# Performance work log

Hardware: AMD Instinct MI355X
Metric: run time of the kernel (lower is better)

The kernel has to match this reference:

```python
import math
import jax, jax.numpy as jnp
import numpy as np

C, H, W, N = 128, 64, 64, 32


def setup_inputs() -> dict:
    key = jax.random.key(0)
    k = jax.random.split(key, 6)
    std = 0.02
    return {
        "x": jax.random.normal(k[0], (N, C, H, W), dtype=jnp.float32),
        # p_3: 1x1 conv, weight [out=C, in=3C]
        "w3": jax.random.normal(k[1], (C, 3 * C), dtype=jnp.float32) * std,
        "p5_w": jax.random.normal(k[2], (1, 1, H, W), dtype=jnp.float32) * std,
        # p_6: conv (3,1), dilation (3,1), weight [O=C, I=C, 3, 1]
        "w6": jax.random.normal(k[3], (C, C, 3, 1), dtype=jnp.float32) * std,
        "p8_w": jax.random.normal(k[4], (1, C, 1, 1), dtype=jnp.float32) * std,
        "p12_w": jax.random.normal(k[5], (1, 1, 3, H, 1), dtype=jnp.float32) * std,
    }


def reference(x, w3, p5_w, w6, p8_w, p12_w):
    n, c, h, w = x.shape
    # F.unfold(x, (1,3), dilation=(1,2), padding=(0,2)) -> taps at w-2, w, w+2 (zero padded)
    xp = jnp.pad(x, ((0, 0), (0, 0), (0, 0), (2, 2)))
    t1 = jnp.stack([xp[..., 0:w], xp[..., 2:w + 2], xp[..., 4:w + 4]], axis=2)  # [n,c,3,h,w]
    t2 = t1.max(axis=2)                                                          # [n,c,h,w]
    # p_3: 1x1 conv over 3c channels
    t3 = jnp.einsum('nkhw,ok->nohw', t1.reshape(n, c * 3, h, w), w3)            # [n,c,h,w]
    t4 = jnp.maximum(t3[:, :, None], t1)                                         # [n,c,3,h,w]
    t5 = p5_w * t2
    # p_6: (3,1) conv, dilation (3,1), padding (3,0) -> same spatial size
    t6 = jax.lax.conv_general_dilated(
        t5, w6, window_strides=(1, 1), padding=((3, 3), (0, 0)),
        rhs_dilation=(3, 1), dimension_numbers=('NCHW', 'OIHW', 'NCHW'))         # [n,c,h,w]
    t7 = jnp.maximum(x, t6)
    t8 = p8_w * t7
    # bmm: [n,c,hw] x [n,hw,3c] -> [n,c,3c]
    t9 = jnp.einsum('ncp,nkp->nck', t8.reshape(n, c, h * w),
                    t1.reshape(n, c * 3, h * w)) / math.sqrt(h * w)
    t10 = t7[:, :, None] + t4                                                    # [n,c,3,h,w]
    t11 = jnp.maximum(t6[:, :, None], t10)                                       # [n,c,3,h,w]
    t12 = p12_w * t11
    # bmm: [n,hw,3c] x [n,3c,c] -> [n,hw,c]
    t13 = jnp.einsum('nkp,nck->npc', t12.reshape(n, c * 3, h * w), t9) / math.sqrt(c * 3)
    return t13.reshape(n, h, w, c).transpose(0, 3, 1, 2)                         # [n,c,h,w]
```

## Files before the change

### kernel.cpp

```cpp
#include <hip/hip_runtime.h>

#define C_   128
#define P_   4096
#define K3   384
#define CP   (C_*P_)
#define NB_  32

typedef __attribute__((ext_vector_type(8))) short short8;
typedef __attribute__((ext_vector_type(4))) short short4v;
typedef __attribute__((ext_vector_type(4))) float f32x4;

__device__ __forceinline__ short f2bf(float f) {
  union { float f; unsigned u; } v; v.f = f;
  unsigned r = v.u + 0x7fffu + ((v.u >> 16) & 1u);
  return (short)(r >> 16);
}
__device__ __forceinline__ float bf2f(short b) {
  union { unsigned u; float f; } v; v.u = ((unsigned)(unsigned short)b) << 16;
  return v.f;
}
__device__ __forceinline__ void gl_lds16(const void* g, void* l) {
  __builtin_amdgcn_global_load_lds(
      (const __attribute__((address_space(1))) unsigned int*)g,
      (__attribute__((address_space(3))) unsigned int*)l, 16, 0, 0);
}

__global__ __launch_bounds__(256) void prep_kernel(const float* __restrict__ w3,
                                                   const float* __restrict__ w6,
                                                   short* __restrict__ w3p,
                                                   short* __restrict__ w6p) {
  int idx = blockIdx.x * 256 + threadIdx.x;
  int m = idx / K3, kp = idx - m * K3;
  int j = kp >> 7, c = kp & 127;
  w3p[idx] = f2bf(w3[m * K3 + c * 3 + j]);
  w6p[idx] = f2bf(w6[m * K3 + c * 3 + j]);
}

__global__ __launch_bounds__(256) void xk_kernel(const float* __restrict__ x,
                                                 short* __restrict__ xb,
                                                 short* __restrict__ xT) {
  int b = blockIdx.x;
  int pt = b & 63, ct = (b >> 6) & 1, n = b >> 7;
  int p0 = pt * 64, c0 = ct * 64;
  const float* xn = x + (size_t)n * CP;
  short* xbn = xb + (size_t)n * CP;
  short* xTn = xT + (size_t)n * CP;
  __shared__ short Ls[64][68];
  int tid = threadIdx.x;
#pragma unroll
  for (int it = 0; it < 4; ++it) {
    int fid = tid + it * 256;
    int i = fid >> 4, j4 = fid & 15;
    f32x4 v = *(const f32x4*)(xn + (c0 + i) * P_ + p0 + j4 * 4);
    short4v s;
#pragma unroll
    for (int r = 0; r < 4; ++r) s[r] = f2bf(v[r]);
    *(short4v*)(xbn + (c0 + i) * P_ + p0 + j4 * 4) = s;
    *(short4v*)(&Ls[i][j4 * 4]) = s;
  }
  __syncthreads();
#pragma unroll
  for (int it = 0; it < 4; ++it) {
    int oid = tid + it * 256;
    int pr = oid >> 4, cg = oid & 15, cb = cg * 4;
    short4v a;
#pragma unroll
    for (int r = 0; r < 4; ++r) a[r] = Ls[cb + r][pr];
    *(short4v*)(xTn + (p0 + pr) * C_ + c0 + cb) = a;
  }
}

__global__ __launch_bounds__(256) void g12_kernel(const short* __restrict__ w3p,
                                                  const short* __restrict__ w6p,
                                                  const float* __restrict__ p5,
                                                  const short* __restrict__ xT,
                                                  short* __restrict__ t3T,
                                                  short* __restrict__ t6T,
                                                  short* __restrict__ t7T) {
  int blk = blockIdx.x;
  int role = blk & 1;
  int b = blk >> 1;
  int n = b >> 5, pt = b & 31, p0 = pt * 128;
  int tid = threadIdx.x, lane = tid & 63, wv = tid >> 6;
  int wm = (wv & 1) * 64, wp = (wv >> 1) * 64;
  const short* Ap = role ? w3p : w6p;
  const short* xTn = xT + (size_t)n * CP;
  __shared__ __align__(16) short As[4][128][8];
  __shared__ __align__(16) short Bs[4][128][8];
  f32x4 acc[4][4] = {};
  for (int ks = 0; ks < 12; ++ks) {
    int k0 = ks * 32;
    int jr = ks >> 2;
    __syncthreads();
#pragma unroll
    for (int it = 0; it < 2; ++it) {
      int slot = tid + it * 256;
      int q = slot >> 7, m = slot & 127;
      gl_lds16(Ap + m * K3 + k0 + q * 8, &As[q][m][0]);
    }
#pragma unroll
    for (int it = 0; it < 2; ++it) {
      int slot = tid + it * 256;
      int q = slot & 3, pc = slot >> 2;
      int p = p0 + pc;
      int c0k = ((ks & 3) * 32) + q * 8;
      short8 zero = {};
      short8 v;
      if (role) {
        int d = 2 * (jr - 1);
        int wd = (p & 63) + d;
        bool valid = (wd >= 0 && wd < 64);
        int prc = min(max(p + d, 0), P_ - 1);
        v = *(const short8*)(xTn + (size_t)prc * C_ + c0k);
        if (!valid) v = zero;
      } else {
        int pr = p + 192 * (jr - 1);
        bool rv = (pr >= 0 && pr < P_);
        int prc = min(max(pr, 0), P_ - 1);
        int w2 = prc & 63;
        const short* rb = xTn + (size_t)prc * C_ + c0k;
        short8 vm = *(const short8*)rb;
        short8 vl = (w2 >= 2) ? *(const short8*)(rb - 2 * C_) : zero;
        short8 vr = (w2 < 62) ? *(const short8*)(rb + 2 * C_) : zero;
        float p5v = p5[prc];
#pragma unroll
        for (int jj = 0; jj < 8; ++jj)
          v[jj] = f2bf(p5v * fmaxf(fmaxf(bf2f(vl[jj]), bf2f(vm[jj])), bf2f(vr[jj])));
        if (!rv) v = zero;
      }
      *(short8*)(&Bs[q][pc][0]) = v;
    }
    __syncthreads();
    int row = lane & 15, q = lane >> 4;
    short8 a[4], bb[4];
#pragma unroll
    for (int im = 0; im < 4; ++im) a[im] = *(const short8*)(&As[q][wm + im * 16 + row][0]);
#pragma unroll
    for (int ip = 0; ip < 4; ++ip) bb[ip] = *(const short8*)(&Bs[q][wp + ip * 16 + row][0]);
#pragma unroll
    for (int im = 0; im < 4; ++im)
#pragma unroll
      for (int ip = 0; ip < 4; ++ip)
        acc[im][ip] = __builtin_amdgcn_mfma_f32_16x16x32_bf16(a[im], bb[ip], acc[im][ip], 0, 0, 0);
  }
  int col = lane & 15, rq = lane >> 4;
  if (role) {
    short* t3Tn = t3T + (size_t)n * CP;
#pragma unroll
    for (int im = 0; im < 4; ++im)
#pragma unroll
      for (int ip = 0; ip < 4; ++ip) {
        int m0 = wm + im * 16 + rq * 4;
        int p = p0 + wp + ip * 16 + col;
        short4v s;
#pragma unroll
        for (int r = 0; r < 4; ++r) s[r] = f2bf(acc[im][ip][r]);
        *(short4v*)(t3Tn + (size_t)p * C_ + m0) = s;
      }
  } else {
    short* t6Tn = t6T + (size_t)n * CP;
    short* t7Tn = t7T + (size_t)n * CP;
#pragma unroll
    for (int im = 0; im < 4; ++im)
#pragma unroll
      for (int ip = 0; ip < 4; ++ip) {
        int m0 = wm + im * 16 + rq * 4;
        int p = p0 + wp + ip * 16 + col;
        short4v ax = *(const short4v*)(xTn + (size_t)p * C_ + m0);
        short4v s6, s7;
#pragma unroll
        for (int r = 0; r < 4; ++r) {
          float t6v = acc[im][ip][r];
          float t7v = fmaxf(bf2f(ax[r]), t6v);
          s6[r] = f2bf(t6v);
          s7[r] = f2bf(t7v);
        }
        *(short4v*)(t6Tn + (size_t)p * C_ + m0) = s6;
        *(short4v*)(t7Tn + (size_t)p * C_ + m0) = s7;
      }
  }
}

__global__ __launch_bounds__(256) void g3_kernel(const short* __restrict__ xb,
                                                 const short* __restrict__ t7T,
                                                 float* __restrict__ t9) {
  int blk = blockIdx.x;
  int nb = blk % 3;
  int tmp = blk / 3;
  int n = tmp & 31, sk = tmp >> 5;
  int d = 2 * (nb - 1);
  int tid = threadIdx.x, lane = tid & 63, wv = tid >> 6;
  int wm = (wv & 1) * 64, wp = (wv >> 1) * 64;
  const short* xbn = xb + (size_t)n * CP;
  const short* t7n = t7T + (size_t)n * CP;
  __shared__ __align__(16) short As[4][128][8];
  __shared__ __align__(16) short Bs[4][128][8];
  f32x4 acc[4][4] = {};
  for (int ks = 0; ks < 16; ++ks) {
    int pp0 = sk * 512 + ks * 32;
    __syncthreads();
#pragma unroll
    for (int it = 0; it < 2; ++it) {
      int slot = tid + it * 256;
      int q = slot >> 7, kc = slot & 127;
      int pb = pp0 + q * 8;
      const int* src = (const int*)(xbn + kc * P_ + pb + d);
      union { int i[4]; short8 s; } u;
#pragma unroll
      for (int t = 0; t < 4; ++t) u.i[t] = src[t];
      short8 v = u.s;
      int w0 = pb & 63;
      if (nb == 0) { if (w0 == 0) { v[0] = 0; v[1] = 0; } }
      else if (nb == 2) { if (w0 == 56) { v[6] = 0; v[7] = 0; } }
      *(short8*)(&As[q][kc][0]) = v;
    }
#pragma unroll
    for (int it = 0; it < 2; ++it) {
      int slot = tid + it * 256;
      int q = slot >> 7, cc = slot & 127;
      const short* bp = t7n + (size_t)(pp0 + q * 8) * C_ + cc;
      short8 v;
#pragma unroll
      for (int j = 0; j < 8; ++j) v[j] = bp[j * C_];
      *(short8*)(&Bs[q][cc][0]) = v;
    }
    __syncthreads();
    int row = lane & 15, q = lane >> 4;
    short8 a[4], bb[4];
#pragma unroll
    for (int im = 0; im < 4; ++im) a[im] = *(const short8*)(&As[q][wm + im * 16 + row][0]);
#pragma unroll
    for (int ip = 0; ip < 4; ++ip) bb[ip] = *(const short8*)(&Bs[q][wp + ip * 16 + row][0]);
#pragma unroll
    for (int im = 0; im < 4; ++im)
#pragma unroll
      for (int ip = 0; ip < 4; ++ip)
        acc[im][ip] = __builtin_amdgcn_mfma_f32_16x16x32_bf16(a[im], bb[ip], acc[im][ip], 0, 0, 0);
  }
  int col = lane & 15, rq = lane >> 4;
  float* t9n = t9 + (size_t)n * (K3 * C_);
#pragma unroll
  for (int im = 0; im < 4; ++im)
#pragma unroll
    for (int ip = 0; ip < 4; ++ip)
#pragma unroll
      for (int r = 0; r < 4; ++r) {
        int kp = nb * 128 + wm + im * 16 + rq * 4 + r;
        int c = wp + ip * 16 + col;
        atomicAdd(&t9n[(size_t)kp * C_ + c], acc[im][ip][r]);
      }
}

__global__ __launch_bounds__(256) void g4_kernel(const float* __restrict__ t9,
                                                 const float* __restrict__ p8,
                                                 const float* __restrict__ p12,
                                                 const short* __restrict__ t3T,
                                                 const short* __restrict__ t6T,
                                                 const short* __restrict__ t7T,
                                                 const short* __restrict__ xT,
                                                 float* __restrict__ out) {
  int b = blockIdx.x;
  int n = b >> 5, pt = b & 31, p0 = pt * 128;
  int tid = threadIdx.x, lane = tid & 63, wv = tid >> 6;
  int wm = (wv & 1) * 64, wp = (wv >> 1) * 64;
  const float* t9n = t9 + (size_t)n * (K3 * C_);
  const short* t3n = t3T + (size_t)n * CP;
  const short* t6n = t6T + (size_t)n * CP;
  const short* t7n = t7T + (size_t)n * CP;
  const short* xTn = xT + (size_t)n * CP;
  const float INV = 1.0f / (64.0f * 19.5959179423f);
  __shared__ __align__(16) short As[4][128][8];
  __shared__ __align__(16) short Bs[4][128][8];
  f32x4 acc[4][4] = {};
  for (int ks = 0; ks < 12; ++ks) {
    int k0 = ks * 32;
    int j = ks >> 2, d = 2 * (j - 1);
    __syncthreads();
#pragma unroll
    for (int it = 0; it < 2; ++it) {
      int slot = tid + it * 256;
      int q = slot >> 7, m = slot & 127;
      float sc = p8[m] * INV;
      short8 v;
#pragma unroll
      for (int jj = 0; jj < 8; ++jj)
        v[jj] = f2bf(t9n[(size_t)(k0 + q * 8 + jj) * C_ + m] * sc);
      *(short8*)(&As[q][m][0]) = v;
    }
#pragma unroll
    for (int it = 0; it < 2; ++it) {
      int slot = tid + it * 256;
      int q = slot & 3, pc = slot >> 2;
      int p = p0 + pc;
      int c0k = ((ks & 3) * 32) + q * 8;
      float s12 = p12[j * 64 + (p >> 6)];
      size_t base = (size_t)p * C_ + c0k;
      short8 a6 = *(const short8*)(t6n + base);
      short8 a7 = *(const short8*)(t7n + base);
      short8 a3 = *(const short8*)(t3n + base);
      int wd = (p & 63) + d;
      bool valid = (wd >= 0 && wd < 64);
      int pr = min(max(p + d, 0), P_ - 1);
      short8 ax = *(const short8*)(xTn + (size_t)pr * C_ + c0k);
      short8 zero = {};
      if (!valid) ax = zero;
      short8 v;
#pragma unroll
      for (int jj = 0; jj < 8; ++jj) {
        float t11 = fmaxf(bf2f(a6[jj]), bf2f(a7[jj]) + fmaxf(bf2f(a3[jj]), bf2f(ax[jj])));
        v[jj] = f2bf(s12 * t11);
      }
      *(short8*)(&Bs[q][pc][0]) = v;
    }
    __syncthreads();
    int row = lane & 15, q = lane >> 4;
    short8 a[4], bb[4];
#pragma unroll
    for (int im = 0; im < 4; ++im) a[im] = *(const short8*)(&As[q][wm + im * 16 + row][0]);
#pragma unroll
    for (int ip = 0; ip < 4; ++ip) bb[ip] = *(const short8*)(&Bs[q][wp + ip * 16 + row][0]);
#pragma unroll
    for (int im = 0; im < 4; ++im)
#pragma unroll
      for (int ip = 0; ip < 4; ++ip)
        acc[im][ip] = __builtin_amdgcn_mfma_f32_16x16x32_bf16(a[im], bb[ip], acc[im][ip], 0, 0, 0);
  }
  int col = lane & 15, rq = lane >> 4;
#pragma unroll
  for (int im = 0; im < 4; ++im)
#pragma unroll
    for (int ip = 0; ip < 4; ++ip)
#pragma unroll
      for (int r = 0; r < 4; ++r) {
        int m = wm + im * 16 + rq * 4 + r;
        int p = p0 + wp + ip * 16 + col;
        out[(size_t)n * CP + m * P_ + p] = acc[im][ip][r];
      }
}

extern "C" void kernel_launch(void* const* d_in, const int* in_sizes, int n_in,
                              void* d_out, int out_size, void* d_ws, size_t ws_size,
                              hipStream_t stream) {
  const float* x   = (const float*)d_in[0];
  const float* w3  = (const float*)d_in[1];
  const float* p5  = (const float*)d_in[2];
  const float* w6  = (const float*)d_in[3];
  const float* p8  = (const float*)d_in[4];
  const float* p12 = (const float*)d_in[5];
  float* out = (float*)d_out;

  char* ws = (char*)d_ws;
  const size_t RB = (size_t)NB_ * CP * 2;
  size_t off = 256;
  short* xb  = (short*)(ws + off); off += RB;
  short* xT  = (short*)(ws + off); off += RB;
  short* t3T = (short*)(ws + off); off += RB;
  short* t6T = (short*)(ws + off); off += RB;
  short* t7T = (short*)(ws + off); off += RB;
  float* t9  = (float*)(ws + off); off += (size_t)NB_ * K3 * C_ * 4;
  short* w3p = (short*)(ws + off); off += 49152 * 2;
  short* w6p = (short*)(ws + off); off += 49152 * 2;

  prep_kernel<<<192, 256, 0, stream>>>(w3, w6, w3p, w6p);
  xk_kernel<<<4096, 256, 0, stream>>>(x, xb, xT);
  g12_kernel<<<2048, 256, 0, stream>>>(w3p, w6p, p5, xT, t3T, t6T, t7T);
  hipMemsetAsync(t9, 0, (size_t)NB_ * K3 * C_ * sizeof(float), stream);
  g3_kernel<<<768, 256, 0, stream>>>(xb, t7T, t9);
  g4_kernel<<<1024, 256, 0, stream>>>(t9, p8, p12, t3T, t6T, t7T, xT, out);
}
```

Before: 447.8 us.

## Double-buffer LDS in GEMM kernels and pre-transpose t9 to bf16

```diff
diff --git a/kernel.cpp b/kernel.cpp
--- a/kernel.cpp
+++ b/kernel.cpp
@@ -85,63 +85,92 @@
   int wm = (wv & 1) * 64, wp = (wv >> 1) * 64;
   const short* Ap = role ? w3p : w6p;
   const short* xTn = xT + (size_t)n * CP;
-  __shared__ __align__(16) short As[4][128][8];
-  __shared__ __align__(16) short Bs[4][128][8];
+  __shared__ __align__(16) short As[2][4][128][8];
+  __shared__ __align__(16) short Bs[2][4][128][8];
   f32x4 acc[4][4] = {};
-  for (int ks = 0; ks < 12; ++ks) {
-    int k0 = ks * 32;
+  short8 bm[2], bl[2], br[2];
+  float bp5[2];
+
+  auto stageA = [&](int ks, int bf) {
+#pragma unroll
+    for (int it = 0; it < 2; ++it) {
+      int slot = tid + it * 256;
+      int q = slot >> 7, m = slot & 127;
+      gl_lds16(Ap + m * K3 + ks * 32 + q * 8, &As[bf][q][m][0]);
+    }
+  };
+  auto loadB = [&](int ks) {
     int jr = ks >> 2;
-    __syncthreads();
-#pragma unroll
-    for (int it = 0; it < 2; ++it) {
-      int slot = tid + it * 256;
-      int q = slot >> 7, m = slot & 127;
-      gl_lds16(Ap + m * K3 + k0 + q * 8, &As[q][m][0]);
-    }
 #pragma unroll
     for (int it = 0; it < 2; ++it) {
       int slot = tid + it * 256;
       int q = slot & 3, pc = slot >> 2;
       int p = p0 + pc;
       int c0k = ((ks & 3) * 32) + q * 8;
+      if (role) {
+        int d = 2 * (jr - 1);
+        int prc = min(max(p + d, 0), P_ - 1);
+        bm[it] = *(const short8*)(xTn + (size_t)prc * C_ + c0k);
+      } else {
+        int pr = p + 192 * (jr - 1);
+        int prc = min(max(pr, 0), P_ - 1);
+        int w2 = prc & 63;
+        const short* rb = xTn + (size_t)prc * C_ + c0k;
+        short8 zero = {};
+        bm[it] = *(const short8*)rb;
+        bl[it] = (w2 >= 2) ? *(const short8*)(rb - 2 * C_) : zero;
+        br[it] = (w2 < 62) ? *(const short8*)(rb + 2 * C_) : zero;
+        bp5[it] = p5[prc];
+      }
+    }
+  };
+  auto writeB = [&](int ks, int bf) {
+    int jr = ks >> 2;
+#pragma unroll
+    for (int it = 0; it < 2; ++it) {
+      int slot = tid + it * 256;
+      int q = slot & 3, pc = slot >> 2;
+      int p = p0 + pc;
       short8 zero = {};
       short8 v;
       if (role) {
         int d = 2 * (jr - 1);
         int wd = (p & 63) + d;
-        bool valid = (wd >= 0 && wd < 64);
-        int prc = min(max(p + d, 0), P_ - 1);
-        v = *(const short8*)(xTn + (size_t)prc * C_ + c0k);
-        if (!valid) v = zero;
+        v = bm[it];
+        if (!(wd >= 0 && wd < 64)) v = zero;
       } else {
         int pr = p + 192 * (jr - 1);
         bool rv = (pr >= 0 && pr < P_);
-        int prc = min(max(pr, 0), P_ - 1);
-        int w2 = prc & 63;
-        const short* rb = xTn + (size_t)prc * C_ + c0k;
-        short8 vm = *(const short8*)rb;
-        short8 vl = (w2 >= 2) ? *(const short8*)(rb - 2 * C_) : zero;
-        short8 vr = (w2 < 62) ? *(const short8*)(rb + 2 * C_) : zero;
-        float p5v = p5[prc];
 #pragma unroll
         for (int jj = 0; jj < 8; ++jj)
-          v[jj] = f2bf(p5v * fmaxf(fmaxf(bf2f(vl[jj]), bf2f(vm[jj])), bf2f(vr[jj])));
+          v[jj] = f2bf(bp5[it] * fmaxf(fmaxf(bf2f(bl[it][jj]), bf2f(bm[it][jj])), bf2f(br[it][jj])));
         if (!rv) v = zero;
       }
-      *(short8*)(&Bs[q][pc][0]) = v;
-    }
-    __syncthreads();
+      *(short8*)(&Bs[bf][q][pc][0]) = v;
+    }
+  };
+
+  stageA(0, 0);
+  loadB(0);
+  writeB(0, 0);
+  __syncthreads();
+#pragma unroll 2
+  for (int ks = 0; ks < 12; ++ks) {
+    int cur = ks & 1, nxt = cur ^ 1;
+    if (ks < 11) { stageA(ks + 1, nxt); loadB(ks + 1); }
     int row = lane & 15, q = lane >> 4;
     short8 a[4], bb[4];
 #pragma unroll
-    for (int im = 0; im < 4; ++im) a[im] = *(const short8*)(&As[q][wm + im * 16 + row][0]);
-#pragma unroll
-    for (int ip = 0; ip < 4; ++ip) bb[ip] = *(const short8*)(&Bs[q][wp + ip * 16 + row][0]);
+    for (int im = 0; im < 4; ++im) a[im] = *(const short8*)(&As[cur][q][wm + im * 16 + row][0]);
+#pragma unroll
+    for (int ip = 0; ip < 4; ++ip) bb[ip] = *(const short8*)(&Bs[cur][q][wp + ip * 16 + row][0]);
 #pragma unroll
     for (int im = 0; im < 4; ++im)
 #pragma unroll
       for (int ip = 0; ip < 4; ++ip)
         acc[im][ip] = __builtin_amdgcn_mfma_f32_16x16x32_bf16(a[im], bb[ip], acc[im][ip], 0, 0, 0);
+    if (ks < 11) writeB(ks + 1, nxt);
+    __syncthreads();
   }
   int col = lane & 15, rq = lane >> 4;
   if (role) {
@@ -193,49 +222,66 @@
   int wm = (wv & 1) * 64, wp = (wv >> 1) * 64;
   const short* xbn = xb + (size_t)n * CP;
   const short* t7n = t7T + (size_t)n * CP;
-  __shared__ __align__(16) short As[4][128][8];
-  __shared__ __align__(16) short Bs[4][128][8];
+  __shared__ __align__(16) short As[2][4][128][8];
+  __shared__ __align__(16) short Bs[2][4][128][8];
   f32x4 acc[4][4] = {};
-  for (int ks = 0; ks < 16; ++ks) {
+  short8 av[2], bv[2];
+
+  auto loadAB = [&](int ks) {
     int pp0 = sk * 512 + ks * 32;
-    __syncthreads();
-#pragma unroll
-    for (int it = 0; it < 2; ++it) {
-      int slot = tid + it * 256;
-      int q = slot >> 7, kc = slot & 127;
+#pragma unroll
+    for (int it = 0; it < 2; ++it) {
+      int slot = tid + it * 256;
+      int q = slot >> 7, rr = slot & 127;
       int pb = pp0 + q * 8;
-      const int* src = (const int*)(xbn + kc * P_ + pb + d);
+      const int* src = (const int*)(xbn + rr * P_ + pb + d);
       union { int i[4]; short8 s; } u;
 #pragma unroll
       for (int t = 0; t < 4; ++t) u.i[t] = src[t];
-      short8 v = u.s;
+      av[it] = u.s;
+      const short* bp = t7n + (size_t)pb * C_ + rr;
+      short8 w;
+#pragma unroll
+      for (int j = 0; j < 8; ++j) w[j] = bp[j * C_];
+      bv[it] = w;
+    }
+  };
+  auto writeAB = [&](int ks, int bf) {
+    int pp0 = sk * 512 + ks * 32;
+#pragma unroll
+    for (int it = 0; it < 2; ++it) {
+      int slot = tid + it * 256;
+      int q = slot >> 7, rr = slot & 127;
+      int pb = pp0 + q * 8;
+      short8 v = av[it];
       int w0 = pb & 63;
       if (nb == 0) { if (w0 == 0) { v[0] = 0; v[1] = 0; } }
       else if (nb == 2) { if (w0 == 56) { v[6] = 0; v[7] = 0; } }
-      *(short8*)(&As[q][kc][0]) = v;
-    }
-#pragma unroll
-    for (int it = 0; it < 2; ++it) {
-      int slot = tid + it * 256;
-      int q = slot >> 7, cc = slot & 127;
-      const short* bp = t7n + (size_t)(pp0 + q * 8) * C_ + cc;
-      short8 v;
-#pragma unroll
-      for (int j = 0; j < 8; ++j) v[j] = bp[j * C_];
-      *(short8*)(&Bs[q][cc][0]) = v;
-    }
-    __syncthreads();
+      *(short8*)(&As[bf][q][rr][0]) = v;
+      *(short8*)(&Bs[bf][q][rr][0]) = bv[it];
+    }
+  };
+
+  loadAB(0);
+  writeAB(0, 0);
+  __syncthreads();
+#pragma unroll 2
+  for (int ks = 0; ks < 16; ++ks) {
+    int cur = ks & 1, nxt = cur ^ 1;
+    if (ks < 15) loadAB(ks + 1);
     int row = lane & 15, q = lane >> 4;
     short8 a[4], bb[4];
 #pragma unroll
-    for (int im = 0; im < 4; ++im) a[im] = *(const short8*)(&As[q][wm + im * 16 + row][0]);
-#pragma unroll
-    for (int ip = 0; ip < 4; ++ip) bb[ip] = *(const short8*)(&Bs[q][wp + ip * 16 + row][0]);
+    for (int im = 0; im < 4; ++im) a[im] = *(const short8*)(&As[cur][q][wm + im * 16 + row][0]);
+#pragma unroll
+    for (int ip = 0; ip < 4; ++ip) bb[ip] = *(const short8*)(&Bs[cur][q][wp + ip * 16 + row][0]);
 #pragma unroll
     for (int im = 0; im < 4; ++im)
 #pragma unroll
       for (int ip = 0; ip < 4; ++ip)
         acc[im][ip] = __builtin_amdgcn_mfma_f32_16x16x32_bf16(a[im], bb[ip], acc[im][ip], 0, 0, 0);
+    if (ks < 15) writeAB(ks + 1, nxt);
+    __syncthreads();
   }
   int col = lane & 15, rq = lane >> 4;
   float* t9n = t9 + (size_t)n * (K3 * C_);
@@ -251,8 +297,42 @@
       }
 }
 
-__global__ __launch_bounds__(256) void g4_kernel(const float* __restrict__ t9,
-                                                 const float* __restrict__ p8,
+__global__ __launch_bounds__(256) void t9s_kernel(const float* __restrict__ t9,
+                                                  const float* __restrict__ p8,
+                                                  short* __restrict__ t9b) {
+  int b = blockIdx.x;
+  int n = b / 6, kt = b - n * 6;
+  int k0 = kt * 64;
+  const float INV = 1.0f / (64.0f * 19.5959179423f);
+  const float* t9n = t9 + (size_t)n * (K3 * C_);
+  short* t9bn = t9b + (size_t)n * (C_ * K3);
+  __shared__ float L[64][132];
+  int tid = threadIdx.x;
+#pragma unroll
+  for (int it = 0; it < 8; ++it) {
+    int s = tid + it * 256;
+    int k = s >> 5, c4 = s & 31;
+    f32x4 v = *(const f32x4*)(t9n + (size_t)(k0 + k) * C_ + c4 * 4);
+    *(f32x4*)(&L[k][c4 * 4]) = v;
+  }
+  __syncthreads();
+#pragma unroll
+  for (int it = 0; it < 2; ++it) {
+    int s = tid + it * 256;
+    int c = s >> 2, kg = s & 3;
+    float sc = p8[c] * INV;
+    short8 o0, o1;
+#pragma unroll
+    for (int j = 0; j < 8; ++j) o0[j] = f2bf(L[kg * 16 + j][c] * sc);
+#pragma unroll
+    for (int j = 0; j < 8; ++j) o1[j] = f2bf(L[kg * 16 + 8 + j][c] * sc);
+    short* op = t9bn + (size_t)c * K3 + k0 + kg * 16;
+    *(short8*)(op) = o0;
+    *(short8*)(op + 8) = o1;
+  }
+}
+
+__global__ __launch_bounds__(256) void g4_kernel(const short* __restrict__ t9b,
                                                  const float* __restrict__ p12,
                                                  const short* __restrict__ t3T,
                                                  const short* __restrict__ t6T,
@@ -263,67 +343,86 @@
   int n = b >> 5, pt = b & 31, p0 = pt * 128;
   int tid = threadIdx.x, lane = tid & 63, wv = tid >> 6;
   int wm = (wv & 1) * 64, wp = (wv >> 1) * 64;
-  const float* t9n = t9 + (size_t)n * (K3 * C_);
+  const short* t9n = t9b + (size_t)n * (K3 * C_);
   const short* t3n = t3T + (size_t)n * CP;
   const short* t6n = t6T + (size_t)n * CP;
   const short* t7n = t7T + (size_t)n * CP;
   const short* xTn = xT + (size_t)n * CP;
-  const float INV = 1.0f / (64.0f * 19.5959179423f);
-  __shared__ __align__(16) short As[4][128][8];
-  __shared__ __align__(16) short Bs[4][128][8];
+  __shared__ __align__(16) short As[2][4][128][8];
+  __shared__ __align__(16) short Bs[2][4][128][8];
   f32x4 acc[4][4] = {};
-  for (int ks = 0; ks < 12; ++ks) {
-    int k0 = ks * 32;
+  short8 r6[2], r7[2], r3[2], rx[2];
+  float rs12[2];
+
+  auto stageA = [&](int ks, int bf) {
+#pragma unroll
+    for (int it = 0; it < 2; ++it) {
+      int slot = tid + it * 256;
+      int q = slot >> 7, m = slot & 127;
+      gl_lds16(t9n + (size_t)m * K3 + ks * 32 + q * 8, &As[bf][q][m][0]);
+    }
+  };
+  auto loadB = [&](int ks) {
     int j = ks >> 2, d = 2 * (j - 1);
-    __syncthreads();
-#pragma unroll
-    for (int it = 0; it < 2; ++it) {
-      int slot = tid + it * 256;
-      int q = slot >> 7, m = slot & 127;
-      float sc = p8[m] * INV;
-      short8 v;
-#pragma unroll
-      for (int jj = 0; jj < 8; ++jj)
-        v[jj] = f2bf(t9n[(size_t)(k0 + q * 8 + jj) * C_ + m] * sc);
-      *(short8*)(&As[q][m][0]) = v;
-    }
+    int k0c = (ks & 3) * 32;
 #pragma unroll
     for (int it = 0; it < 2; ++it) {
       int slot = tid + it * 256;
       int q = slot & 3, pc = slot >> 2;
       int p = p0 + pc;
-      int c0k = ((ks & 3) * 32) + q * 8;
-      float s12 = p12[j * 64 + (p >> 6)];
+      int c0k = k0c + q * 8;
       size_t base = (size_t)p * C_ + c0k;
-      short8 a6 = *(const short8*)(t6n + base);
-      short8 a7 = *(const short8*)(t7n + base);
-      short8 a3 = *(const short8*)(t3n + base);
+      r6[it] = *(const short8*)(t6n + base);
+      r7[it] = *(const short8*)(t7n + base);
+      r3[it] = *(const short8*)(t3n + base);
+      int pr = min(max(p + d, 0), P_ - 1);
+      rx[it] = *(const short8*)(xTn + (size_t)pr * C_ + c0k);
+      rs12[it] = p12[j * 64 + (p >> 6)];
+    }
+  };
+  auto writeB = [&](int ks, int bf) {
+    int j = ks >> 2, d = 2 * (j - 1);
+#pragma unroll
+    for (int it = 0; it < 2; ++it) {
+      int slot = tid + it * 256;
+      int q = slot & 3, pc = slot >> 2;
+      int p = p0 + pc;
       int wd = (p & 63) + d;
       bool valid = (wd >= 0 && wd < 64);
-      int pr = min(max(p + d, 0), P_ - 1);
-      short8 ax = *(const short8*)(xTn + (size_t)pr * C_ + c0k);
       short8 zero = {};
+      short8 ax = rx[it];
       if (!valid) ax = zero;
       short8 v;
 #pragma unroll
       for (int jj = 0; jj < 8; ++jj) {
-        float t11 = fmaxf(bf2f(a6[jj]), bf2f(a7[jj]) + fmaxf(bf2f(a3[jj]), bf2f(ax[jj])));
-        v[jj] = f2bf(s12 * t11);
-      }
-      *(short8*)(&Bs[q][pc][0]) = v;
-    }
-    __syncthreads();
+        float t11 = fmaxf(bf2f(r6[it][jj]), bf2f(r7[it][jj]) + fmaxf(bf2f(r3[it][jj]), bf2f(ax[jj])));
+        v[jj] = f2bf(rs12[it] * t11);
+      }
+      *(short8*)(&Bs[bf][q][pc][0]) = v;
+    }
+  };
+
+  stageA(0, 0);
+  loadB(0);
+  writeB(0, 0);
+  __syncthreads();
+#pragma unroll 2
+  for (int ks = 0; ks < 12; ++ks) {
+    int cur = ks & 1, nxt = cur ^ 1;
+    if (ks < 11) { stageA(ks + 1, nxt); loadB(ks + 1); }
     int row = lane & 15, q = lane >> 4;
     short8 a[4], bb[4];
 #pragma unroll
-    for (int im = 0; im < 4; ++im) a[im] = *(const short8*)(&As[q][wm + im * 16 + row][0]);
-#pragma unroll
-    for (int ip = 0; ip < 4; ++ip) bb[ip] = *(const short8*)(&Bs[q][wp + ip * 16 + row][0]);
+    for (int im = 0; im < 4; ++im) a[im] = *(const short8*)(&As[cur][q][wm + im * 16 + row][0]);
+#pragma unroll
+    for (int ip = 0; ip < 4; ++ip) bb[ip] = *(const short8*)(&Bs[cur][q][wp + ip * 16 + row][0]);
 #pragma unroll
     for (int im = 0; im < 4; ++im)
 #pragma unroll
       for (int ip = 0; ip < 4; ++ip)
         acc[im][ip] = __builtin_amdgcn_mfma_f32_16x16x32_bf16(a[im], bb[ip], acc[im][ip], 0, 0, 0);
+    if (ks < 11) writeB(ks + 1, nxt);
+    __syncthreads();
   }
   int col = lane & 15, rq = lane >> 4;
 #pragma unroll
@@ -360,11 +459,13 @@
   float* t9  = (float*)(ws + off); off += (size_t)NB_ * K3 * C_ * 4;
   short* w3p = (short*)(ws + off); off += 49152 * 2;
   short* w6p = (short*)(ws + off); off += 49152 * 2;
+  short* t9b = xb;
 
   prep_kernel<<<192, 256, 0, stream>>>(w3, w6, w3p, w6p);
   xk_kernel<<<4096, 256, 0, stream>>>(x, xb, xT);
   g12_kernel<<<2048, 256, 0, stream>>>(w3p, w6p, p5, xT, t3T, t6T, t7T);
   hipMemsetAsync(t9, 0, (size_t)NB_ * K3 * C_ * sizeof(float), stream);
   g3_kernel<<<768, 256, 0, stream>>>(xb, t7T, t9);
-  g4_kernel<<<1024, 256, 0, stream>>>(t9, p8, p12, t3T, t6T, t7T, xT, out);
-}
+  t9s_kernel<<<192, 256, 0, stream>>>(t9, p8, t9b);
+  g4_kernel<<<1024, 256, 0, stream>>>(t9b, p12, t3T, t6T, t7T, xT, out);
+}
```

Measured after the change: 475.0 us. 1.06x slower.
